# Optimization experiments

Hardware: AMD Instinct MI355X
Metric: run time of the kernel (lower is better)

The kernel has to match this reference:

```python
import jax, jax.numpy as jnp
import numpy as np

D_MODEL = 1024
NUM_EXPERTS = 64
TOP_K = 2
N_TOKENS = 131072


def setup_inputs() -> dict:
    key = jax.random.key(0)
    kx, kw, kb = jax.random.split(key, 3)
    x = jax.random.normal(kx, (N_TOKENS, D_MODEL), dtype=jnp.float32)
    # nn.Linear(input_dim, num_experts): weight [E, D], bias [E]
    W = jax.random.normal(kw, (NUM_EXPERTS, D_MODEL), dtype=jnp.float32) * (1.0 / np.sqrt(D_MODEL))
    b = jax.random.normal(kb, (NUM_EXPERTS,), dtype=jnp.float32) * 0.01
    return {"x": x, "W": W, "b": b}


def reference(x, W, b):
    # logits = x @ W.T + b  -> [N, E]
    logits = jnp.einsum("nd,ed->ne", x, W) + b
    topk_vals, topk_idx = jax.lax.top_k(logits, TOP_K)          # [N, k]
    gate_w = jax.nn.softmax(topk_vals, axis=-1)                  # [N, k]
    rows = jnp.arange(logits.shape[0])[:, None]                  # [N, 1]
    sparse = jnp.zeros_like(logits).at[rows, topk_idx].set(gate_w)
    return sparse
```

## Files before the change

kernel.cpp:

```cpp
#include <hip/hip_runtime.h>
#include <math.h>


#define D_MODEL 1024
#define N_EXP   64
#define NSTEP   32
#define BLOCK   256
#define TOK_PER_WAVE  32
#define TOK_PER_BLOCK 128
#define NTILE   2

typedef float  f32x4 __attribute__((ext_vector_type(4)));
typedef __bf16 bf16x8 __attribute__((ext_vector_type(8)));

__global__ __launch_bounds__(256) void wprep_kernel(
    const float* __restrict__ W, __bf16* __restrict__ WH, __bf16* __restrict__ WL)
{
    const int tid = blockIdx.x * 256 + threadIdx.x;
    const int s = tid >> 8;
    const int g = (tid >> 6) & 3;
    const int l = tid & 63;
    const int e  = g * 16 + (l & 15);
    const int k0 = s * 32 + ((l >> 4) & 3) * 8;
    const float* __restrict__ src = W + (size_t)e * D_MODEL + k0;
    bf16x8 h, lo;
#pragma unroll
    for (int i = 0; i < 8; ++i) {
        const float f = src[i];
        const __bf16 hh = (__bf16)f;
        h[i]  = hh;
        lo[i] = (__bf16)(f - (float)hh);
    }
    reinterpret_cast<bf16x8*>(WH)[tid] = h;
    reinterpret_cast<bf16x8*>(WL)[tid] = lo;
}

__global__ __launch_bounds__(BLOCK, 4) void gating_kernel(
    const float* __restrict__ x,
    const __bf16* __restrict__ WH,
    const __bf16* __restrict__ WL,
    const float* __restrict__ b,
    float* __restrict__ out,
    int n_tokens)
{
    __shared__ f32x4 info[4 * TOK_PER_WAVE];

    const int tid = threadIdx.x;
    const int w   = tid >> 6;
    const int l   = tid & 63;
    const int cl  = l & 15;
    const int rg  = (l >> 4) & 3;

    const int wtok0 = blockIdx.x * TOK_PER_BLOCK + w * TOK_PER_WAVE;

    const bf16x8* __restrict__ WHv = reinterpret_cast<const bf16x8*>(WH);
    const bf16x8* __restrict__ WLv = reinterpret_cast<const bf16x8*>(WL);

    f32x4 acc[NTILE][4];
#pragma unroll
    for (int g = 0; g < 4; ++g) {
        const f32x4 bi = *reinterpret_cast<const f32x4*>(b + g * 16 + rg * 4);
#pragma unroll
        for (int t = 0; t < NTILE; ++t) acc[t][g] = bi;
    }

    const float* xrow[NTILE];
#pragma unroll
    for (int t = 0; t < NTILE; ++t) {
        int tk = wtok0 + t * 16 + cl;
        tk = tk < n_tokens ? tk : (n_tokens - 1);
        xrow[t] = x + (size_t)tk * D_MODEL + rg * 8;
    }

    f32x4 xa[NTILE][2], xb[NTILE][2];
    bf16x8 wh[4], wl[4];

#define LOADX(BUF, S)                                                         \
    _Pragma("unroll")                                                         \
    for (int t = 0; t < NTILE; ++t) {                                         \
        const float* p = xrow[t] + (S) * 32;                                  \
        BUF[t][0] = *reinterpret_cast<const f32x4*>(p);                       \
        BUF[t][1] = *reinterpret_cast<const f32x4*>(p + 4);                   \
    }
#define LOADW(S)                                                              \
    _Pragma("unroll")                                                         \
    for (int g = 0; g < 4; ++g) {                                             \
        wh[g] = WHv[((S) * 4 + g) * 64 + l];                                  \
        wl[g] = WLv[((S) * 4 + g) * 64 + l];                                  \
    }
#define PROC(XB)                                                              \
    _Pragma("unroll")                                                         \
    for (int t = 0; t < NTILE; ++t) {                                         \
        bf16x8 bh, bl;                                                        \
        _Pragma("unroll")                                                     \
        for (int i = 0; i < 8; ++i) {                                         \
            const float f = (i < 4) ? XB[t][0][i] : XB[t][1][i - 4];          \
            const __bf16 hh = (__bf16)f;                                      \
            bh[i] = hh;                                                       \
            bl[i] = (__bf16)(f - (float)hh);                                  \
        }                                                                     \
        _Pragma("unroll")                                                     \
        for (int g = 0; g < 4; ++g) {                                         \
            f32x4 c = acc[t][g];                                              \
            c = __builtin_amdgcn_mfma_f32_16x16x32_bf16(wh[g], bh, c, 0, 0, 0); \
            c = __builtin_amdgcn_mfma_f32_16x16x32_bf16(wh[g], bl, c, 0, 0, 0); \
            c = __builtin_amdgcn_mfma_f32_16x16x32_bf16(wl[g], bh, c, 0, 0, 0); \
            acc[t][g] = c;                                                    \
        }                                                                     \
    }

    LOADX(xa, 0);
    for (int s = 0; s < NSTEP; s += 2) {
        LOADW(s);
        LOADX(xb, s + 1);
        PROC(xa);
        LOADW(s + 1);
        if (s + 2 < NSTEP) { LOADX(xa, s + 2); }
        PROC(xb);
    }
#undef LOADX
#undef LOADW
#undef PROC

    const int wbase = w * TOK_PER_WAVE;
#pragma unroll
    for (int t = 0; t < NTILE; ++t) {
        float m1 = -INFINITY, m2 = -INFINITY;
        int i1 = 0, i2 = 0;
#pragma unroll
        for (int g = 0; g < 4; ++g) {
#pragma unroll
            for (int r = 0; r < 4; ++r) {
                const float v = acc[t][g][r];
                const int e = g * 16 + rg * 4 + r;
                if (v > m1)      { m2 = m1; i2 = i1; m1 = v; i1 = e; }
                else if (v > m2) { m2 = v;  i2 = e; }
            }
        }
#pragma unroll
        for (int d = 16; d <= 32; d <<= 1) {
            const float om1 = __shfl_xor(m1, d, 64);
            const int   oi1 = __shfl_xor(i1, d, 64);
            const float om2 = __shfl_xor(m2, d, 64);
            const int   oi2 = __shfl_xor(i2, d, 64);
            const bool  sw  = om1 > m1;
            const float a1 = sw ? om1 : m1; const int ai1 = sw ? oi1 : i1;
            const float cc = sw ? m1  : om1; const int ci = sw ? i1  : oi1;
            const float dd = sw ? om2 : m2;  const int di = sw ? oi2 : i2;
            const bool  sw2 = dd > cc;
            m1 = a1; i1 = ai1;
            m2 = sw2 ? dd : cc; i2 = sw2 ? di : ci;
        }
        const float e2 = expf(m2 - m1);
        const float g1 = 1.0f / (1.0f + e2);
        const float g2 = e2 * g1;
        if (rg == 0) {
            f32x4 q;
            q[0] = __int_as_float(i1);
            q[1] = __int_as_float(i2);
            q[2] = g1;
            q[3] = g2;
            info[wbase + t * 16 + cl] = q;
        }
    }

#pragma unroll
    for (int j = 0; j < TOK_PER_WAVE / 4; ++j) {
        const int row = j * 4 + rg;
        const f32x4 q = info[wbase + row];
        const int I1 = __float_as_int(q[0]);
        const int I2 = __float_as_int(q[1]);
        const float G1 = q[2], G2 = q[3];
        const int e0 = cl * 4;
        f32x4 o;
#pragma unroll
        for (int c = 0; c < 4; ++c) {
            const int e = e0 + c;
            o[c] = (e == I1) ? G1 : ((e == I2) ? G2 : 0.0f);
        }
        const int tokg = wtok0 + row;
        if (tokg < n_tokens) {
            reinterpret_cast<f32x4*>(out + (size_t)tokg * N_EXP)[cl] = o;
        }
    }
}

extern "C" void kernel_launch(void* const* d_in, const int* in_sizes, int n_in,
                              void* d_out, int out_size, void* d_ws, size_t ws_size,
                              hipStream_t stream) {
    const float* x = (const float*)d_in[0];
    const float* W = (const float*)d_in[1];
    const float* b = (const float*)d_in[2];
    float* out = (float*)d_out;

    const int n_tokens = in_sizes[0] / D_MODEL;

    __bf16* WH = (__bf16*)d_ws;
    __bf16* WL = WH + (size_t)N_EXP * D_MODEL;

    wprep_kernel<<<32, 256, 0, stream>>>(W, WH, WL);

    const int grid = (n_tokens + TOK_PER_BLOCK - 1) / TOK_PER_BLOCK;
    gating_kernel<<<grid, BLOCK, 0, stream>>>(x, WH, WL, b, out, n_tokens);
}
```

Before: 731.9 us.

## Stage x tiles through double-buffered swizzled LDS with coalesced row loads

Each block now loads 128 tokens by 64 floats per chunk from global memory, with contiguous 16-byte segments per row, into a double-buffered XOR-swizzled LDS tile. Waves then read their MFMA operands from LDS instead of issuing strided per-lane global loads of 32-byte pieces. This is meant to improve global load coalescing and overlap the next chunk's fetch with MFMA work. In exchange it adds 64 KB of LDS, a block-wide barrier per chunk, and lowers the launch-bounds occupancy hint from 4 to 2 blocks per CU.

```diff
diff --git a/kernel.cpp b/kernel.cpp
--- a/kernel.cpp
+++ b/kernel.cpp
@@ -9,6 +9,8 @@
 #define TOK_PER_WAVE  32
 #define TOK_PER_BLOCK 128
 #define NTILE   2
+#define NCHUNK  16
+#define CH_BYTES 2048
 
 typedef float  f32x4 __attribute__((ext_vector_type(4)));
 typedef __bf16 bf16x8 __attribute__((ext_vector_type(8)));
@@ -35,7 +37,7 @@
     reinterpret_cast<bf16x8*>(WL)[tid] = lo;
 }
 
-__global__ __launch_bounds__(BLOCK, 4) void gating_kernel(
+__global__ __launch_bounds__(BLOCK, 2) void gating_kernel(
     const float* __restrict__ x,
     const __bf16* __restrict__ WH,
     const __bf16* __restrict__ WL,
@@ -43,6 +45,7 @@
     float* __restrict__ out,
     int n_tokens)
 {
+    __shared__ char  xs[2][16 * CH_BYTES];
     __shared__ f32x4 info[4 * TOK_PER_WAVE];
 
     const int tid = threadIdx.x;
@@ -51,7 +54,8 @@
     const int cl  = l & 15;
     const int rg  = (l >> 4) & 3;
 
-    const int wtok0 = blockIdx.x * TOK_PER_BLOCK + w * TOK_PER_WAVE;
+    const int btok  = blockIdx.x * TOK_PER_BLOCK;
+    const int wtok0 = btok + w * TOK_PER_WAVE;
 
     const bf16x8* __restrict__ WHv = reinterpret_cast<const bf16x8*>(WH);
     const bf16x8* __restrict__ WLv = reinterpret_cast<const bf16x8*>(WL);
@@ -64,63 +68,80 @@
         for (int t = 0; t < NTILE; ++t) acc[t][g] = bi;
     }
 
-    const float* xrow[NTILE];
-#pragma unroll
-    for (int t = 0; t < NTILE; ++t) {
-        int tk = wtok0 + t * 16 + cl;
-        tk = tk < n_tokens ? tk : (n_tokens - 1);
-        xrow[t] = x + (size_t)tk * D_MODEL + rg * 8;
-    }
-
-    f32x4 xa[NTILE][2], xb[NTILE][2];
-    bf16x8 wh[4], wl[4];
-
-#define LOADX(BUF, S)                                                         \
+    f32x4 U[8];
+    bf16x8 wha[4], wla[4], whb[4], wlb[4];
+
+#define STAGE_LOAD(C)                                                         \
+    _Pragma("unroll")                                                         \
+    for (int i = 0; i < 8; ++i) {                                             \
+        const int gg = i * BLOCK + tid;                                       \
+        const int srow = gg >> 4, sch = gg & 15;                              \
+        int tk = btok + srow; tk = tk < n_tokens ? tk : (n_tokens - 1);       \
+        U[i] = *reinterpret_cast<const f32x4*>(                               \
+            x + (size_t)tk * D_MODEL + (C) * 64 + sch * 4);                   \
+    }
+#define STAGE_WRITE(BUF)                                                      \
+    _Pragma("unroll")                                                         \
+    for (int i = 0; i < 8; ++i) {                                             \
+        const int gg = i * BLOCK + tid;                                       \
+        const int srow = gg >> 4, sch = gg & 15;                              \
+        *reinterpret_cast<f32x4*>(                                            \
+            xs[BUF] + sch * CH_BYTES + ((srow ^ (sch & 7)) << 4)) = U[i];     \
+    }
+#define LOADW(WH_, WL_, S)                                                    \
+    _Pragma("unroll")                                                         \
+    for (int g = 0; g < 4; ++g) {                                             \
+        WH_[g] = WHv[((S) * 4 + g) * 64 + l];                                 \
+        WL_[g] = WLv[((S) * 4 + g) * 64 + l];                                 \
+    }
+#define PROCQ(BUF, Q, WH_, WL_)                                               \
     _Pragma("unroll")                                                         \
     for (int t = 0; t < NTILE; ++t) {                                         \
-        const float* p = xrow[t] + (S) * 32;                                  \
-        BUF[t][0] = *reinterpret_cast<const f32x4*>(p);                       \
-        BUF[t][1] = *reinterpret_cast<const f32x4*>(p + 4);                   \
-    }
-#define LOADW(S)                                                              \
-    _Pragma("unroll")                                                         \
-    for (int g = 0; g < 4; ++g) {                                             \
-        wh[g] = WHv[((S) * 4 + g) * 64 + l];                                  \
-        wl[g] = WLv[((S) * 4 + g) * 64 + l];                                  \
-    }
-#define PROC(XB)                                                              \
-    _Pragma("unroll")                                                         \
-    for (int t = 0; t < NTILE; ++t) {                                         \
+        const int row = w * TOK_PER_WAVE + t * 16 + cl;                       \
         bf16x8 bh, bl;                                                        \
         _Pragma("unroll")                                                     \
-        for (int i = 0; i < 8; ++i) {                                         \
-            const float f = (i < 4) ? XB[t][0][i] : XB[t][1][i - 4];          \
-            const __bf16 hh = (__bf16)f;                                      \
-            bh[i] = hh;                                                       \
-            bl[i] = (__bf16)(f - (float)hh);                                  \
+        for (int hf = 0; hf < 2; ++hf) {                                      \
+            const int ch = (Q) * 8 + rg * 2 + hf;                             \
+            const f32x4 xf = *reinterpret_cast<const f32x4*>(                 \
+                xs[BUF] + ch * CH_BYTES + ((row ^ (ch & 7)) << 4));           \
+            _Pragma("unroll")                                                 \
+            for (int ii = 0; ii < 4; ++ii) {                                  \
+                const float f = xf[ii];                                       \
+                const __bf16 hv = (__bf16)f;                                  \
+                bh[hf * 4 + ii] = hv;                                         \
+                bl[hf * 4 + ii] = (__bf16)(f - (float)hv);                    \
+            }                                                                 \
         }                                                                     \
         _Pragma("unroll")                                                     \
         for (int g = 0; g < 4; ++g) {                                         \
             f32x4 c = acc[t][g];                                              \
-            c = __builtin_amdgcn_mfma_f32_16x16x32_bf16(wh[g], bh, c, 0, 0, 0); \
-            c = __builtin_amdgcn_mfma_f32_16x16x32_bf16(wh[g], bl, c, 0, 0, 0); \
-            c = __builtin_amdgcn_mfma_f32_16x16x32_bf16(wl[g], bh, c, 0, 0, 0); \
+            c = __builtin_amdgcn_mfma_f32_16x16x32_bf16(WH_[g], bh, c, 0, 0, 0); \
+            c = __builtin_amdgcn_mfma_f32_16x16x32_bf16(WH_[g], bl, c, 0, 0, 0); \
+            c = __builtin_amdgcn_mfma_f32_16x16x32_bf16(WL_[g], bh, c, 0, 0, 0); \
             acc[t][g] = c;                                                    \
         }                                                                     \
     }
 
-    LOADX(xa, 0);
-    for (int s = 0; s < NSTEP; s += 2) {
-        LOADW(s);
-        LOADX(xb, s + 1);
-        PROC(xa);
-        LOADW(s + 1);
-        if (s + 2 < NSTEP) { LOADX(xa, s + 2); }
-        PROC(xb);
-    }
-#undef LOADX
+    STAGE_LOAD(0);
+    STAGE_WRITE(0);
+    __syncthreads();
+
+    for (int c = 0; c < NCHUNK; ++c) {
+        const int cur = c & 1;
+        LOADW(wha, wla, 2 * c);
+        LOADW(whb, wlb, 2 * c + 1);
+        if (c + 1 < NCHUNK) STAGE_LOAD(c + 1);
+        PROCQ(cur, 0, wha, wla);
+        PROCQ(cur, 1, whb, wlb);
+        if (c + 1 < NCHUNK) {
+            STAGE_WRITE(cur ^ 1);
+            __syncthreads();
+        }
+    }
+#undef STAGE_LOAD
+#undef STAGE_WRITE
 #undef LOADW
-#undef PROC
+#undef PROCQ
 
     const int wbase = w * TOK_PER_WAVE;
 #pragma unroll
@@ -174,9 +195,9 @@
         const int e0 = cl * 4;
         f32x4 o;
 #pragma unroll
-        for (int c = 0; c < 4; ++c) {
-            const int e = e0 + c;
-            o[c] = (e == I1) ? G1 : ((e == I2) ? G2 : 0.0f);
+        for (int ccx = 0; ccx < 4; ++ccx) {
+            const int e = e0 + ccx;
+            o[ccx] = (e == I1) ? G1 : ((e == I2) ? G2 : 0.0f);
         }
         const int tokg = wtok0 + row;
         if (tokg < n_tokens) {
```

New measurement: 725.9 us. About the same (-0.8%).
